# Kernel optimization log

Hardware: AMD Instinct MI355X
Metric: run time of the kernel (lower is better)

## Reference

```python
import jax, jax.numpy as jnp
import numpy as np

N_NODES = 100000

def _mean_aggregate(h, edge_index, num_nodes):
    # PyG convention: edge_index[0]=source j, edge_index[1]=target i; mean over in-neighbors
    src, dst = edge_index[0], edge_index[1]
    summed = jax.ops.segment_sum(h[src], dst, num_segments=num_nodes)  # [N, D]
    cnt = jax.ops.segment_sum(jnp.ones((src.shape[0],), h.dtype), dst, num_segments=num_nodes)
    return summed / jnp.maximum(cnt, 1.0)[:, None]

def _sage_conv(h, edge_index, Wl, bl, Wr, num_nodes):
    agg = _mean_aggregate(h, edge_index, num_nodes)
    return agg @ Wl.T + bl + h @ Wr.T

def setup_inputs() -> dict:
    key = jax.random.key(0)
    ks = jax.random.split(key, 12)
    D = 64
    scale = 1.0 / np.sqrt(D)
    x = jax.random.normal(ks[0], (N_NODES, D), jnp.float32)
    edge_index = jax.random.randint(ks[1], (2, 1000000), 0, N_NODES, jnp.int32)
    edge_label_index = jax.random.randint(ks[2], (2, 200000), 0, N_NODES, jnp.int32)
    def w(k):
        return (jax.random.normal(k, (D, D), jnp.float32) * scale)
    return {
        'x': x,
        'edge_index': edge_index,
        'edge_label_index': edge_label_index,
        'W_lin': w(ks[3]), 'b_lin': jnp.zeros((D,), jnp.float32),
        'Wl1': w(ks[4]), 'bl1': jnp.zeros((D,), jnp.float32), 'Wr1': w(ks[5]),
        'Wl2': w(ks[6]), 'bl2': jnp.zeros((D,), jnp.float32), 'Wr2': w(ks[7]),
    }

def reference(x, edge_index, edge_label_index, W_lin, b_lin, Wl1, bl1, Wr1, Wl2, bl2, Wr2):
    h = x @ W_lin.T + b_lin                                   # node_lin
    h = jax.nn.relu(_sage_conv(h, edge_index, Wl1, bl1, Wr1, N_NODES))  # conv1 + relu
    h = _sage_conv(h, edge_index, Wl2, bl2, Wr2, N_NODES)               # conv2
    # edge dot-product classifier
    preds = jnp.sum(h[edge_label_index[0]] * h[edge_label_index[1]], axis=-1)  # [E_label]
    return preds
```

## Files before the change

kernel.cpp:

```cpp
#include <hip/hip_runtime.h>

#define DD 64
#define BW 512
#define NBMAX 256
#define CAPB 8192
#define CHUNK 2048

typedef unsigned short u16;
typedef unsigned char u8;
typedef u16 ushort8v __attribute__((ext_vector_type(8)));
typedef short s16x8 __attribute__((ext_vector_type(8)));
typedef float f32x4 __attribute__((ext_vector_type(4)));
typedef float f32x2 __attribute__((ext_vector_type(2)));

__device__ __forceinline__ float bf2f(u16 u) {
    union { unsigned u32; float f; } x; x.u32 = (unsigned)u << 16; return x.f;
}
__device__ __forceinline__ u16 f2bf(float f) {
    union { float f; unsigned u; } x; x.f = f;
    unsigned r = (x.u + 0x7fffu + ((x.u >> 16) & 1u)) >> 16;
    return (u16)r;
}
__device__ __forceinline__ u8 f2fp8(float v) {
    return (u8)(__builtin_amdgcn_cvt_pk_fp8_f32(v, v, 0, false) & 0xff);
}

#define ACC16(u) do { \
    f32x2 _p; \
    _p = __builtin_amdgcn_cvt_pk_f32_fp8((int)(u).x, false); a[0]  += _p[0]; a[1]  += _p[1]; \
    _p = __builtin_amdgcn_cvt_pk_f32_fp8((int)(u).x, true);  a[2]  += _p[0]; a[3]  += _p[1]; \
    _p = __builtin_amdgcn_cvt_pk_f32_fp8((int)(u).y, false); a[4]  += _p[0]; a[5]  += _p[1]; \
    _p = __builtin_amdgcn_cvt_pk_f32_fp8((int)(u).y, true);  a[6]  += _p[0]; a[7]  += _p[1]; \
    _p = __builtin_amdgcn_cvt_pk_f32_fp8((int)(u).z, false); a[8]  += _p[0]; a[9]  += _p[1]; \
    _p = __builtin_amdgcn_cvt_pk_f32_fp8((int)(u).z, true);  a[10] += _p[0]; a[11] += _p[1]; \
    _p = __builtin_amdgcn_cvt_pk_f32_fp8((int)(u).w, false); a[12] += _p[0]; a[13] += _p[1]; \
    _p = __builtin_amdgcn_cvt_pk_f32_fp8((int)(u).w, true);  a[14] += _p[0]; a[15] += _p[1]; \
} while (0)

__global__ void k_part(const int* __restrict__ ei, int n_edges,
                       int* __restrict__ fill, unsigned* __restrict__ part,
                       const float* __restrict__ w0, const float* __restrict__ w1,
                       const float* __restrict__ w2, const float* __restrict__ w3,
                       const float* __restrict__ w4, u16* __restrict__ wb) {
    __shared__ int hist[NBMAX];
    __shared__ int curs[NBMAX];
    int t = threadIdx.x;
    {
        int i = blockIdx.x * 256 + t;
        if (i < 5 * DD * DD) {
            int mat = i >> 12, off = i & 4095;
            const float* src = (mat == 0) ? w0 : (mat == 1) ? w1 : (mat == 2) ? w2
                             : (mat == 3) ? w3 : w4;
            wb[i] = f2bf(src[off]);
        }
    }
    hist[t] = 0;
    __syncthreads();
    int c0 = blockIdx.x * CHUNK;
    int c1 = min(n_edges, c0 + CHUNK);
    for (int e = c0 + t; e < c1; e += 256)
        atomicAdd(&hist[ei[n_edges + e] >> 9], 1);
    __syncthreads();
    int base = 0;
    if (hist[t] > 0) base = atomicAdd(&fill[t], hist[t]);
    curs[t] = base;
    __syncthreads();
    for (int e = c0 + t; e < c1; e += 256) {
        int dst = ei[n_edges + e];
        int src = ei[e];
        int b = dst >> 9;
        int pos = atomicAdd(&curs[b], 1);
        if (pos < CAPB)
            part[(size_t)b * CAPB + pos] = ((unsigned)src << 9) | (unsigned)(dst & 511);
    }
}

__global__ __launch_bounds__(256) void k_build(const unsigned* __restrict__ part,
                        const int* __restrict__ fill,
                        int* __restrict__ row_start, int* __restrict__ row_deg,
                        int* __restrict__ csr, int n_nodes) {
    __shared__ int cnt_l[BW];
    __shared__ int sc[BW];
    __shared__ unsigned csr_l[CAPB];
    int t = threadIdx.x;
    int b = blockIdx.x;
    int beg = b * CAPB;
    int size = min(fill[b], CAPB);

    cnt_l[t] = 0; cnt_l[256 + t] = 0;
    __syncthreads();
    for (int j = t; j < size; j += 256)
        atomicAdd(&cnt_l[part[beg + j] & 511], 1);
    __syncthreads();
    int v0 = cnt_l[t], v1 = cnt_l[256 + t];
    sc[t] = v0; sc[256 + t] = v1;
    cnt_l[t] = 0; cnt_l[256 + t] = 0;
    __syncthreads();
    for (int off = 1; off < 256; off <<= 1) {
        int a = (t >= off) ? sc[t - off] : 0;
        int c = (t >= off) ? sc[256 + t - off] : 0;
        __syncthreads();
        if (t >= off) { sc[t] += a; sc[256 + t] += c; }
        __syncthreads();
    }
    int tot0 = sc[255];
    __syncthreads();
    sc[256 + t] += tot0;
    __syncthreads();
    {
        int n0 = b * BW + t;
        if (n0 < n_nodes) {
            row_start[n0] = beg + ((t == 0) ? 0 : sc[t - 1]);
            row_deg[n0] = v0;
        }
        int n1 = b * BW + 256 + t;
        if (n1 < n_nodes) {
            row_start[n1] = beg + sc[255 + t];
            row_deg[n1] = v1;
        }
    }
    for (int j = t; j < size; j += 256) {
        unsigned p = part[beg + j];
        int dl = (int)(p & 511u);
        int pos = ((dl == 0) ? 0 : sc[dl - 1]) + atomicAdd(&cnt_l[dl], 1);
        csr_l[pos] = p >> 9;
    }
    __syncthreads();
    for (int i = t; i < size; i += 256) csr[beg + i] = (int)csr_l[i];
}

__global__ __launch_bounds__(256) void k_lin(
    const float* __restrict__ A, const u16* __restrict__ W,
    const float* __restrict__ bias, u16* __restrict__ out, u8* __restrict__ out8,
    int n_nodes) {
    int t = threadIdx.x;
    int lane = t & 63;
    int col = lane & 15;
    int quad = lane >> 4;
    int m0 = blockIdx.x * 64 + (t >> 6) * 16;
    int arow = m0 + col;
    if (arow > n_nodes - 1) arow = n_nodes - 1;

    f32x4 acc[4];
    #pragma unroll
    for (int nt = 0; nt < 4; ++nt) {
        float bv = bias[nt * 16 + col];
        acc[nt] = (f32x4){bv, bv, bv, bv};
    }
    #pragma unroll
    for (int ks = 0; ks < 2; ++ks) {
        int k0 = ks * 32 + quad * 8;
        const float* p = A + (size_t)arow * DD + k0;
        float4 v0 = *(const float4*)p;
        float4 v1 = *(const float4*)(p + 4);
        s16x8 a;
        a[0] = (short)f2bf(v0.x); a[1] = (short)f2bf(v0.y);
        a[2] = (short)f2bf(v0.z); a[3] = (short)f2bf(v0.w);
        a[4] = (short)f2bf(v1.x); a[5] = (short)f2bf(v1.y);
        a[6] = (short)f2bf(v1.z); a[7] = (short)f2bf(v1.w);
        #pragma unroll
        for (int nt = 0; nt < 4; ++nt) {
            s16x8 b = *(const s16x8*)(W + (nt * 16 + col) * DD + k0);
            acc[nt] = __builtin_amdgcn_mfma_f32_16x16x32_bf16(a, b, acc[nt], 0, 0, 0);
        }
    }
    int mbase = m0 + quad * 4;
    #pragma unroll
    for (int nt = 0; nt < 4; ++nt)
        #pragma unroll
        for (int i = 0; i < 4; ++i) {
            int m = mbase + i;
            if (m < n_nodes) {
                float v = acc[nt][i];
                out[(size_t)m * DD + nt * 16 + col] = f2bf(v);
                out8[(size_t)m * DD + nt * 16 + col] = f2fp8(v);
            }
        }
}

__global__ __launch_bounds__(256) void k_conv(
    const u16* __restrict__ h, const u8* __restrict__ h8,
    const int* __restrict__ row_start, const int* __restrict__ row_deg,
    const int* __restrict__ csr,
    const u16* __restrict__ Wl, const u16* __restrict__ Wr,
    const float* __restrict__ bias, u16* __restrict__ out, u8* __restrict__ out8,
    int n_nodes, int relu) {
    __shared__ u16 mean_l[64 * DD];
    int t = threadIdx.x;
    int w = t >> 6, lane = t & 63;
    int nn = lane >> 2;
    int r = lane & 3;
    int m0 = blockIdx.x * 64;

    {
        int li = w * 16 + nn;
        int n = m0 + li;
        int beg = 0, end = 0;
        if (n < n_nodes) { beg = row_start[n]; end = beg + row_deg[n]; }
        float a[16];
        #pragma unroll
        for (int kk = 0; kk < 16; ++kk) a[kk] = 0.f;
        int j = beg;
        for (; j + 3 < end; j += 4) {
            int s0 = csr[j], s1 = csr[j + 1], s2 = csr[j + 2], s3 = csr[j + 3];
            uint4 u0 = *(const uint4*)(h8 + (size_t)s0 * DD + r * 16);
            uint4 u1 = *(const uint4*)(h8 + (size_t)s1 * DD + r * 16);
            uint4 u2 = *(const uint4*)(h8 + (size_t)s2 * DD + r * 16);
            uint4 u3 = *(const uint4*)(h8 + (size_t)s3 * DD + r * 16);
            ACC16(u0); ACC16(u1); ACC16(u2); ACC16(u3);
        }
        for (; j < end; ++j) {
            uint4 u0 = *(const uint4*)(h8 + (size_t)csr[j] * DD + r * 16);
            ACC16(u0);
        }
        int deg = end - beg;
        float inv = (deg > 0) ? 1.0f / (float)deg : 0.0f;
        ushort8v o0, o1;
        #pragma unroll
        for (int kk = 0; kk < 8; ++kk) { o0[kk] = f2bf(a[kk] * inv); o1[kk] = f2bf(a[8 + kk] * inv); }
        *(ushort8v*)(mean_l + li * DD + r * 16) = o0;
        *(ushort8v*)(mean_l + li * DD + r * 16 + 8) = o1;
    }
    __threadfence_block();

    int col = lane & 15;
    int quad = lane >> 4;
    int arow = m0 + w * 16 + col;
    if (arow > n_nodes - 1) arow = n_nodes - 1;

    f32x4 acc[4];
    #pragma unroll
    for (int nt = 0; nt < 4; ++nt) {
        float bv = bias[nt * 16 + col];
        acc[nt] = (f32x4){bv, bv, bv, bv};
    }
    #pragma unroll
    for (int ks = 0; ks < 2; ++ks) {
        int k0 = ks * 32 + quad * 8;
        s16x8 am = *(const s16x8*)(mean_l + (w * 16 + col) * DD + k0);
        s16x8 ah = *(const s16x8*)(h + (size_t)arow * DD + k0);
        #pragma unroll
        for (int nt = 0; nt < 4; ++nt) {
            s16x8 bl = *(const s16x8*)(Wl + (nt * 16 + col) * DD + k0);
            acc[nt] = __builtin_amdgcn_mfma_f32_16x16x32_bf16(am, bl, acc[nt], 0, 0, 0);
            s16x8 br = *(const s16x8*)(Wr + (nt * 16 + col) * DD + k0);
            acc[nt] = __builtin_amdgcn_mfma_f32_16x16x32_bf16(ah, br, acc[nt], 0, 0, 0);
        }
    }
    int mbase = m0 + w * 16 + quad * 4;
    #pragma unroll
    for (int nt = 0; nt < 4; ++nt)
        #pragma unroll
        for (int i = 0; i < 4; ++i) {
            int m = mbase + i;
            if (m < n_nodes) {
                float v = acc[nt][i];
                if (relu) v = fmaxf(v, 0.f);
                out[(size_t)m * DD + nt * 16 + col] = f2bf(v);
                if (out8) out8[(size_t)m * DD + nt * 16 + col] = f2fp8(v);
            }
        }
}

__global__ void k_pred(const u16* __restrict__ h, const int* __restrict__ eli,
                       int n_label, float* __restrict__ out) {
    int t = threadIdx.x;
    int e = blockIdx.x * 16 + (t >> 4);
    if (e >= n_label) return;
    int g = (t >> 3) & 1;
    int r = t & 7;
    int node = g ? eli[n_label + e] : eli[e];
    ushort8v v = *(const ushort8v*)(h + (size_t)node * DD + r * 8);
    float s = 0.f;
    #pragma unroll
    for (int kk = 0; kk < 8; ++kk) {
        float f = bf2f(v[kk]);
        s += f * __shfl_xor(f, 8, 64);
    }
    #pragma unroll
    for (int off = 1; off < 8; off <<= 1) s += __shfl_xor(s, off, 64);
    if ((t & 15) == 0) out[e] = s;
}

extern "C" void kernel_launch(void* const* d_in, const int* in_sizes, int n_in,
                              void* d_out, int out_size, void* d_ws, size_t ws_size,
                              hipStream_t stream) {
    const float* x     = (const float*)d_in[0];
    const int*   ei    = (const int*)d_in[1];
    const int*   eli   = (const int*)d_in[2];
    const float* W_lin = (const float*)d_in[3];
    const float* b_lin = (const float*)d_in[4];
    const float* Wl1   = (const float*)d_in[5];
    const float* bl1   = (const float*)d_in[6];
    const float* Wr1   = (const float*)d_in[7];
    const float* Wl2   = (const float*)d_in[8];
    const float* bl2   = (const float*)d_in[9];
    const float* Wr2   = (const float*)d_in[10];

    int n_nodes = in_sizes[0] / DD;
    int n_edges = in_sizes[1] / 2;
    int n_label = in_sizes[2] / 2;
    float* out = (float*)d_out;

    int nb = (n_nodes + BW - 1) / BW;

    char* ws = (char*)d_ws;
    size_t hbytes = (size_t)n_nodes * DD * sizeof(u16);
    u16* hA   = (u16*)ws; ws += hbytes;
    u16* hB   = (u16*)ws; ws += hbytes;
    u8* h8A   = (u8*)ws;  ws += (size_t)n_nodes * DD;
    u8* h8B   = (u8*)ws;  ws += (size_t)n_nodes * DD;
    int* row_start = (int*)ws; ws += (size_t)((n_nodes + 3) & ~3) * sizeof(int);
    int* row_deg   = (int*)ws; ws += (size_t)((n_nodes + 3) & ~3) * sizeof(int);
    int* fill      = (int*)ws; ws += NBMAX * sizeof(int);
    u16* wb        = (u16*)ws; ws += 5 * DD * DD * sizeof(u16);
    unsigned* part = (unsigned*)ws; ws += (size_t)nb * CAPB * sizeof(unsigned);
    int* csr       = (int*)ws; ws += (size_t)nb * CAPB * sizeof(int);

    int nb_chunk = (n_edges + CHUNK - 1) / CHUNK;

    (void)hipMemsetAsync(fill, 0, NBMAX * sizeof(int), stream);
    k_part<<<nb_chunk, 256, 0, stream>>>(ei, n_edges, fill, part, W_lin, Wl1, Wr1, Wl2, Wr2, wb);
    k_build<<<nb, 256, 0, stream>>>(part, fill, row_start, row_deg, csr, n_nodes);

    int nb_gemm = (n_nodes + 63) / 64;
    int nb_pred = (n_label + 15) / 16;

    k_lin<<<nb_gemm, 256, 0, stream>>>(x, wb, b_lin, hA, h8A, n_nodes);

    k_conv<<<nb_gemm, 256, 0, stream>>>(hA, h8A, row_start, row_deg, csr,
                                        wb + 4096, wb + 2 * 4096, bl1, hB, h8B, n_nodes, 1);

    k_conv<<<nb_gemm, 256, 0, stream>>>(hB, h8B, row_start, row_deg, csr,
                                        wb + 3 * 4096, wb + 4 * 4096, bl2, hA, nullptr, n_nodes, 0);

    k_pred<<<nb_pred, 256, 0, stream>>>(hA, eli, n_label, out);
}
```

Measured before the change: 213.7 us.

## Merge edge partitioning and input linear layer into one launch, halve bucket width

Fuses the edge-partition kernel and the node linear layer into a single launch. Blocks below nb_chunk do partitioning and the remaining blocks do the MFMA GEMM, which now converts W_lin from fp32 on the fly instead of reading a pre-converted bf16 copy. This removes a launch and the dependency between the two, so both kinds of work can overlap. The destination bucket width also drops from 512 to 256 nodes (CAPB 4096, more buckets), giving k_build more, smaller blocks. Since each bucket still holds up to 4096 entries, per-bucket overflow becomes more likely under skewed degree distributions.

```diff
diff --git a/kernel.cpp b/kernel.cpp
--- a/kernel.cpp
+++ b/kernel.cpp
@@ -1,9 +1,9 @@
 #include <hip/hip_runtime.h>
 
 #define DD 64
-#define BW 512
-#define NBMAX 256
-#define CAPB 8192
+#define BW 256
+#define NBMAX 512
+#define CAPB 4096
 #define CHUNK 2048
 
 typedef unsigned short u16;
@@ -37,41 +37,102 @@
     _p = __builtin_amdgcn_cvt_pk_f32_fp8((int)(u).w, true);  a[14] += _p[0]; a[15] += _p[1]; \
 } while (0)
 
-__global__ void k_part(const int* __restrict__ ei, int n_edges,
-                       int* __restrict__ fill, unsigned* __restrict__ part,
-                       const float* __restrict__ w0, const float* __restrict__ w1,
-                       const float* __restrict__ w2, const float* __restrict__ w3,
-                       const float* __restrict__ w4, u16* __restrict__ wb) {
-    __shared__ int hist[NBMAX];
-    __shared__ int curs[NBMAX];
+__global__ __launch_bounds__(256) void k_partlin(
+    const int* __restrict__ ei, int n_edges, int nb_chunk,
+    int* __restrict__ fill, unsigned* __restrict__ part,
+    const float* __restrict__ w1, const float* __restrict__ w2,
+    const float* __restrict__ w3, const float* __restrict__ w4,
+    u16* __restrict__ wb,
+    const float* __restrict__ A, const float* __restrict__ W,
+    const float* __restrict__ bias, u16* __restrict__ out, u8* __restrict__ out8,
+    int n_nodes) {
     int t = threadIdx.x;
-    {
-        int i = blockIdx.x * 256 + t;
-        if (i < 5 * DD * DD) {
-            int mat = i >> 12, off = i & 4095;
-            const float* src = (mat == 0) ? w0 : (mat == 1) ? w1 : (mat == 2) ? w2
-                             : (mat == 3) ? w3 : w4;
-            wb[i] = f2bf(src[off]);
-        }
-    }
-    hist[t] = 0;
-    __syncthreads();
-    int c0 = blockIdx.x * CHUNK;
-    int c1 = min(n_edges, c0 + CHUNK);
-    for (int e = c0 + t; e < c1; e += 256)
-        atomicAdd(&hist[ei[n_edges + e] >> 9], 1);
-    __syncthreads();
-    int base = 0;
-    if (hist[t] > 0) base = atomicAdd(&fill[t], hist[t]);
-    curs[t] = base;
-    __syncthreads();
-    for (int e = c0 + t; e < c1; e += 256) {
-        int dst = ei[n_edges + e];
-        int src = ei[e];
-        int b = dst >> 9;
-        int pos = atomicAdd(&curs[b], 1);
-        if (pos < CAPB)
-            part[(size_t)b * CAPB + pos] = ((unsigned)src << 9) | (unsigned)(dst & 511);
+    if ((int)blockIdx.x < nb_chunk) {
+        __shared__ int hist[NBMAX];
+        __shared__ int curs[NBMAX];
+        {
+            int i = blockIdx.x * 256 + t;
+            if (i < 4 * DD * DD) {
+                int mat = i >> 12, off = i & 4095;
+                const float* src = (mat == 0) ? w1 : (mat == 1) ? w2 : (mat == 2) ? w3 : w4;
+                wb[DD * DD + i] = f2bf(src[off]);
+            }
+        }
+        hist[t] = 0; hist[256 + t] = 0;
+        __syncthreads();
+        int c0 = blockIdx.x * CHUNK;
+        int c1 = min(n_edges, c0 + CHUNK);
+        for (int e = c0 + t; e < c1; e += 256)
+            atomicAdd(&hist[ei[n_edges + e] >> 8], 1);
+        __syncthreads();
+        #pragma unroll
+        for (int k = 0; k < 2; ++k) {
+            int idx = k * 256 + t;
+            int h = hist[idx];
+            int base = 0;
+            if (h > 0) base = atomicAdd(&fill[idx], h);
+            curs[idx] = base;
+        }
+        __syncthreads();
+        for (int e = c0 + t; e < c1; e += 256) {
+            int dst = ei[n_edges + e];
+            int src = ei[e];
+            int b = dst >> 8;
+            int pos = atomicAdd(&curs[b], 1);
+            if (pos < CAPB)
+                part[(size_t)b * CAPB + pos] = ((unsigned)src << 8) | (unsigned)(dst & 255);
+        }
+    } else {
+        int bid = (int)blockIdx.x - nb_chunk;
+        int lane = t & 63;
+        int col = lane & 15;
+        int quad = lane >> 4;
+        int m0 = bid * 64 + (t >> 6) * 16;
+        int arow = m0 + col;
+        if (arow > n_nodes - 1) arow = n_nodes - 1;
+
+        f32x4 acc[4];
+        #pragma unroll
+        for (int nt = 0; nt < 4; ++nt) {
+            float bv = bias[nt * 16 + col];
+            acc[nt] = (f32x4){bv, bv, bv, bv};
+        }
+        #pragma unroll
+        for (int ks = 0; ks < 2; ++ks) {
+            int k0 = ks * 32 + quad * 8;
+            const float* p = A + (size_t)arow * DD + k0;
+            float4 v0 = *(const float4*)p;
+            float4 v1 = *(const float4*)(p + 4);
+            s16x8 a;
+            a[0] = (short)f2bf(v0.x); a[1] = (short)f2bf(v0.y);
+            a[2] = (short)f2bf(v0.z); a[3] = (short)f2bf(v0.w);
+            a[4] = (short)f2bf(v1.x); a[5] = (short)f2bf(v1.y);
+            a[6] = (short)f2bf(v1.z); a[7] = (short)f2bf(v1.w);
+            #pragma unroll
+            for (int nt = 0; nt < 4; ++nt) {
+                const float* wp = W + (size_t)(nt * 16 + col) * DD + k0;
+                float4 b0 = *(const float4*)wp;
+                float4 b1 = *(const float4*)(wp + 4);
+                s16x8 bfr;
+                bfr[0] = (short)f2bf(b0.x); bfr[1] = (short)f2bf(b0.y);
+                bfr[2] = (short)f2bf(b0.z); bfr[3] = (short)f2bf(b0.w);
+                bfr[4] = (short)f2bf(b1.x); bfr[5] = (short)f2bf(b1.y);
+                bfr[6] = (short)f2bf(b1.z); bfr[7] = (short)f2bf(b1.w);
+                acc[nt] = __builtin_amdgcn_mfma_f32_16x16x32_bf16(a, bfr, acc[nt], 0, 0, 0);
+            }
+        }
+        int mbase = m0 + quad * 4;
+        #pragma unroll
+        for (int nt = 0; nt < 4; ++nt)
+            #pragma unroll
+            for (int i = 0; i < 4; ++i) {
+                int m = mbase + i;
+                if (m < n_nodes) {
+                    float v = acc[nt][i];
+                    out[(size_t)m * DD + nt * 16 + col] = f2bf(v);
+                    out8[(size_t)m * DD + nt * 16 + col] = f2fp8(v);
+                }
+            }
     }
 }
 
@@ -87,95 +148,36 @@
     int beg = b * CAPB;
     int size = min(fill[b], CAPB);
 
-    cnt_l[t] = 0; cnt_l[256 + t] = 0;
+    cnt_l[t] = 0;
     __syncthreads();
     for (int j = t; j < size; j += 256)
-        atomicAdd(&cnt_l[part[beg + j] & 511], 1);
+        atomicAdd(&cnt_l[part[beg + j] & 255], 1);
     __syncthreads();
-    int v0 = cnt_l[t], v1 = cnt_l[256 + t];
-    sc[t] = v0; sc[256 + t] = v1;
-    cnt_l[t] = 0; cnt_l[256 + t] = 0;
+    int v0 = cnt_l[t];
+    sc[t] = v0;
+    cnt_l[t] = 0;
     __syncthreads();
     for (int off = 1; off < 256; off <<= 1) {
         int a = (t >= off) ? sc[t - off] : 0;
-        int c = (t >= off) ? sc[256 + t - off] : 0;
-        __syncthreads();
-        if (t >= off) { sc[t] += a; sc[256 + t] += c; }
-        __syncthreads();
-    }
-    int tot0 = sc[255];
-    __syncthreads();
-    sc[256 + t] += tot0;
-    __syncthreads();
+        __syncthreads();
+        if (t >= off) sc[t] += a;
+        __syncthreads();
+    }
     {
         int n0 = b * BW + t;
         if (n0 < n_nodes) {
             row_start[n0] = beg + ((t == 0) ? 0 : sc[t - 1]);
             row_deg[n0] = v0;
         }
-        int n1 = b * BW + 256 + t;
-        if (n1 < n_nodes) {
-            row_start[n1] = beg + sc[255 + t];
-            row_deg[n1] = v1;
-        }
     }
     for (int j = t; j < size; j += 256) {
         unsigned p = part[beg + j];
-        int dl = (int)(p & 511u);
+        int dl = (int)(p & 255u);
         int pos = ((dl == 0) ? 0 : sc[dl - 1]) + atomicAdd(&cnt_l[dl], 1);
-        csr_l[pos] = p >> 9;
+        csr_l[pos] = p >> 8;
     }
     __syncthreads();
     for (int i = t; i < size; i += 256) csr[beg + i] = (int)csr_l[i];
-}
-
-__global__ __launch_bounds__(256) void k_lin(
-    const float* __restrict__ A, const u16* __restrict__ W,
-    const float* __restrict__ bias, u16* __restrict__ out, u8* __restrict__ out8,
-    int n_nodes) {
-    int t = threadIdx.x;
-    int lane = t & 63;
-    int col = lane & 15;
-    int quad = lane >> 4;
-    int m0 = blockIdx.x * 64 + (t >> 6) * 16;
-    int arow = m0 + col;
-    if (arow > n_nodes - 1) arow = n_nodes - 1;
-
-    f32x4 acc[4];
-    #pragma unroll
-    for (int nt = 0; nt < 4; ++nt) {
-        float bv = bias[nt * 16 + col];
-        acc[nt] = (f32x4){bv, bv, bv, bv};
-    }
-    #pragma unroll
-    for (int ks = 0; ks < 2; ++ks) {
-        int k0 = ks * 32 + quad * 8;
-        const float* p = A + (size_t)arow * DD + k0;
-        float4 v0 = *(const float4*)p;
-        float4 v1 = *(const float4*)(p + 4);
-        s16x8 a;
-        a[0] = (short)f2bf(v0.x); a[1] = (short)f2bf(v0.y);
-        a[2] = (short)f2bf(v0.z); a[3] = (short)f2bf(v0.w);
-        a[4] = (short)f2bf(v1.x); a[5] = (short)f2bf(v1.y);
-        a[6] = (short)f2bf(v1.z); a[7] = (short)f2bf(v1.w);
-        #pragma unroll
-        for (int nt = 0; nt < 4; ++nt) {
-            s16x8 b = *(const s16x8*)(W + (nt * 16 + col) * DD + k0);
-            acc[nt] = __builtin_amdgcn_mfma_f32_16x16x32_bf16(a, b, acc[nt], 0, 0, 0);
-        }
-    }
-    int mbase = m0 + quad * 4;
-    #pragma unroll
-    for (int nt = 0; nt < 4; ++nt)
-        #pragma unroll
-        for (int i = 0; i < 4; ++i) {
-            int m = mbase + i;
-            if (m < n_nodes) {
-                float v = acc[nt][i];
-                out[(size_t)m * DD + nt * 16 + col] = f2bf(v);
-                out8[(size_t)m * DD + nt * 16 + col] = f2fp8(v);
-            }
-        }
 }
 
 __global__ __launch_bounds__(256) void k_conv(
@@ -318,15 +320,16 @@
     int* csr       = (int*)ws; ws += (size_t)nb * CAPB * sizeof(int);
 
     int nb_chunk = (n_edges + CHUNK - 1) / CHUNK;
-
-    (void)hipMemsetAsync(fill, 0, NBMAX * sizeof(int), stream);
-    k_part<<<nb_chunk, 256, 0, stream>>>(ei, n_edges, fill, part, W_lin, Wl1, Wr1, Wl2, Wr2, wb);
-    k_build<<<nb, 256, 0, stream>>>(part, fill, row_start, row_deg, csr, n_nodes);
-
     int nb_gemm = (n_nodes + 63) / 64;
     int nb_pred = (n_label + 15) / 16;
 
-    k_lin<<<nb_gemm, 256, 0, stream>>>(x, wb, b_lin, hA, h8A, n_nodes);
+    (void)hipMemsetAsync(fill, 0, NBMAX * sizeof(int), stream);
+    k_partlin<<<nb_chunk + nb_gemm, 256, 0, stream>>>(
+        ei, n_edges, nb_chunk, fill, part,
+        Wl1, Wr1, Wl2, Wr2, wb,
+        x, W_lin, b_lin, hA, h8A, n_nodes);
+
+    k_build<<<nb, 256, 0, stream>>>(part, fill, row_start, row_deg, csr, n_nodes);
 
     k_conv<<<nb_gemm, 256, 0, stream>>>(hA, h8A, row_start, row_deg, csr,
                                         wb + 4096, wb + 2 * 4096, bl1, hB, h8B, n_nodes, 1);
```

Measured after the change: 208.1 us. 2.6% less time.
